# Performance work log

Measured on AMD Instinct MI355X. Metric: run time of the kernel, lower is better.

## Reference

```python
import jax, jax.numpy as jnp
import numpy as np

B, D, C = 16384, 512, 1000  # batch, feature dim, number of class prototypes


def setup_inputs() -> dict:
    key = jax.random.key(0)
    kx, kp = jax.random.split(key)
    x = jax.random.normal(kx, (B, D), dtype=jnp.float32)
    protomat = jax.random.normal(kp, (C, D), dtype=jnp.float32)
    return {"x": x, "protomat": protomat}


def reference(x, protomat):
    # Squared L2 distance from every sample to every prototype:
    # dist[b, c] = sum_d (x[b,d] - protomat[c,d])^2
    # materializing the [B, C, D] broadcast the original loop implies.
    x_sq = jnp.sum(x * x, axis=1, keepdims=True)            # [B, 1]
    p_sq = jnp.sum(protomat * protomat, axis=1)             # [C]
    cross = jnp.einsum('bd,cd->bc', x, protomat)            # [B, C]
    return x_sq + p_sq[None, :] - 2.0 * cross               # [B, C]
```

## Files before the change

### kernel.cpp

```cpp
#include <hip/hip_runtime.h>
#include <hip/hip_bf16.h>


#define B_ROWS 16384
#define D_K    512
#define C_COLS 1000
#define C_PAD  1024

#define BM 256
#define BN 256
#define BK 32
#define NK (D_K / BK)
#define NBUF 4
#define TILE_SH 16384

typedef __attribute__((ext_vector_type(8))) short short8;
typedef __attribute__((ext_vector_type(4))) float f32x4;

__device__ __forceinline__ unsigned short f2bf(float f) {
  unsigned u = __float_as_uint(f);
  u += 0x7fffu + ((u >> 16) & 1u);
  return (unsigned short)(u >> 16);
}

__device__ __forceinline__ void gload16(const void* g, void* l) {
  __builtin_amdgcn_global_load_lds(
      (const __attribute__((address_space(1))) unsigned int*)g,
      (__attribute__((address_space(3))) unsigned int*)l, 16, 0, 0);
}

__global__ __launch_bounds__(256) void prep_kernel(
    const float* __restrict__ x, const float* __restrict__ p,
    unsigned short* __restrict__ xb, unsigned short* __restrict__ pb,
    float* __restrict__ xsq, float* __restrict__ psq) {
  const int wave = threadIdx.x >> 6;
  const int lane = threadIdx.x & 63;
  const int row  = blockIdx.x * 4 + wave;
  const bool isx = row < B_ROWS;
  const int r2   = isx ? row : row - B_ROWS;

  float v[8];
  if (isx) {
    const float4* s = reinterpret_cast<const float4*>(x + (size_t)r2 * D_K + lane * 8);
    float4 a = s[0], b = s[1];
    v[0] = a.x; v[1] = a.y; v[2] = a.z; v[3] = a.w;
    v[4] = b.x; v[5] = b.y; v[6] = b.z; v[7] = b.w;
  } else if (r2 < C_COLS) {
    const float4* s = reinterpret_cast<const float4*>(p + (size_t)r2 * D_K + lane * 8);
    float4 a = s[0], b = s[1];
    v[0] = a.x; v[1] = a.y; v[2] = a.z; v[3] = a.w;
    v[4] = b.x; v[5] = b.y; v[6] = b.z; v[7] = b.w;
  } else {
#pragma unroll
    for (int j = 0; j < 8; ++j) v[j] = 0.0f;
  }

  float ss = 0.0f;
  unsigned short u[8];
#pragma unroll
  for (int j = 0; j < 8; ++j) { ss += v[j] * v[j]; u[j] = f2bf(v[j]); }

  uint4 pk;
  pk.x = (unsigned)u[0] | ((unsigned)u[1] << 16);
  pk.y = (unsigned)u[2] | ((unsigned)u[3] << 16);
  pk.z = (unsigned)u[4] | ((unsigned)u[5] << 16);
  pk.w = (unsigned)u[6] | ((unsigned)u[7] << 16);
  unsigned short* dst = (isx ? xb : pb) + (size_t)r2 * D_K + lane * 8;
  *reinterpret_cast<uint4*>(dst) = pk;

#pragma unroll
  for (int off = 32; off > 0; off >>= 1) ss += __shfl_down(ss, off);
  if (lane == 0) (isx ? xsq : psq)[r2] = ss;
}

__global__ __launch_bounds__(512, 2) void gemm_kernel(
    const unsigned short* __restrict__ xb, const unsigned short* __restrict__ pb,
    const float* __restrict__ xsq, const float* __restrict__ psq,
    float* __restrict__ out) {
  __shared__ __align__(16) unsigned short L[NBUF * TILE_SH];

  const int tid  = threadIdx.x;
  const int lane = tid & 63;
  const int wave = tid >> 6;
  const int wm   = wave >> 2;
  const int wn   = wave & 3;

  const int bid = blockIdx.x;
  const int tt  = (bid & 7) * 32 + (bid >> 3);
  const int bm  = tt >> 2;
  const int bn  = tt & 3;

  const int chA0 = tid, chA1 = tid + 512;
  const int rA0 = chA0 >> 2, rA1 = chA1 >> 2;
  const int ksA0 = ((chA0 & 3) - (rA0 >> 1)) & 3;
  const int ksA1 = ((chA1 & 3) - (rA1 >> 1)) & 3;
  const unsigned short* gA0 = xb + ((size_t)bm * BM + rA0) * D_K + ksA0 * 8;
  const unsigned short* gA1 = xb + ((size_t)bm * BM + rA1) * D_K + ksA1 * 8;
  const unsigned short* gB0 = pb + ((size_t)bn * BN + rA0) * D_K + ksA0 * 8;
  const unsigned short* gB1 = pb + ((size_t)bn * BN + rA1) * D_K + ksA1 * 8;
  unsigned short* lA0 = &L[chA0 * 8];
  unsigned short* lA1 = &L[chA1 * 8];
  unsigned short* lB0 = &L[8192 + chA0 * 8];
  unsigned short* lB1 = &L[8192 + chA1 * 8];

  f32x4 acc[8][4];
#pragma unroll
  for (int m = 0; m < 8; ++m)
#pragma unroll
    for (int n = 0; n < 4; ++n) acc[m][n] = (f32x4){0.f, 0.f, 0.f, 0.f};

  const int l15 = lane & 15;
  const int pos = (((lane >> 4) + (l15 >> 1)) & 3);
  const int rdA = (wm * 128 + l15) * 32 + pos * 8;
  const int rdB = 8192 + (wn * 64 + l15) * 32 + pos * 8;

#define STAGE(T, BUF)                                     \
  do {                                                    \
    const int ko = (T)*BK;                                \
    const int bo = (BUF)*TILE_SH;                         \
    gload16(gA0 + ko, lA0 + bo);                          \
    gload16(gA1 + ko, lA1 + bo);                          \
    gload16(gB0 + ko, lB0 + bo);                          \
    gload16(gB1 + ko, lB1 + bo);                          \
  } while (0)

#define COMPUTE(BUF)                                                          \
  do {                                                                        \
    const unsigned short* Ab = &L[(BUF)*TILE_SH] + rdA;                       \
    const unsigned short* Bb = &L[(BUF)*TILE_SH] + rdB;                       \
    short8 bfr[4];                                                            \
    _Pragma("unroll") for (int n = 0; n < 4; ++n)                             \
        bfr[n] = *reinterpret_cast<const short8*>(Bb + n * 512);              \
    __builtin_amdgcn_s_setprio(1);                                            \
    _Pragma("unroll") for (int m = 0; m < 8; ++m) {                           \
      short8 af = *reinterpret_cast<const short8*>(Ab + m * 512);             \
      _Pragma("unroll") for (int n = 0; n < 4; ++n)                           \
          acc[m][n] = __builtin_amdgcn_mfma_f32_16x16x32_bf16(                \
              af, bfr[n], acc[m][n], 0, 0, 0);                                \
    }                                                                         \
    __builtin_amdgcn_s_setprio(0);                                            \
  } while (0)

  STAGE(0, 0);
  STAGE(1, 1);
  STAGE(2, 2);

#pragma unroll 1
  for (int t = 0; t < NK - 3; ++t) {
    asm volatile("s_waitcnt vmcnt(8)" ::: "memory");
    __builtin_amdgcn_s_barrier();
    STAGE(t + 3, (t + 3) & 3);
    COMPUTE(t & 3);
  }
  asm volatile("s_waitcnt vmcnt(8)" ::: "memory");
  __builtin_amdgcn_s_barrier();
  COMPUTE(13 & 3);
  asm volatile("s_waitcnt vmcnt(4)" ::: "memory");
  __builtin_amdgcn_s_barrier();
  COMPUTE(14 & 3);
  asm volatile("s_waitcnt vmcnt(0)" ::: "memory");
  __builtin_amdgcn_s_barrier();
  COMPUTE(15 & 3);

#undef STAGE
#undef COMPUTE

  const int colb = bn * BN + wn * 64 + l15;
  float pc[4];
#pragma unroll
  for (int n = 0; n < 4; ++n) pc[n] = psq[colb + n * 16];

  const int rowb = bm * BM + wm * 128 + ((lane >> 4) << 2);
#pragma unroll
  for (int m = 0; m < 8; ++m) {
#pragma unroll
    for (int r = 0; r < 4; ++r) {
      const int row = rowb + m * 16 + r;
      const float xs = xsq[row];
#pragma unroll
      for (int n = 0; n < 4; ++n) {
        const int c = colb + n * 16;
        if (c < C_COLS)
          out[(size_t)row * C_COLS + c] = xs + pc[n] - 2.0f * acc[m][n][r];
      }
    }
  }
}

extern "C" void kernel_launch(void* const* d_in, const int* in_sizes, int n_in,
                              void* d_out, int out_size, void* d_ws, size_t ws_size,
                              hipStream_t stream) {
  const float* x = (const float*)d_in[0];
  const float* p = (const float*)d_in[1];
  float* out = (float*)d_out;

  char* ws = (char*)d_ws;
  unsigned short* xb  = (unsigned short*)ws;
  unsigned short* pb  = (unsigned short*)(ws + 16777216);
  float* xsq          = (float*)(ws + 16777216 + 1048576);
  float* psq          = (float*)(ws + 16777216 + 1048576 + 65536);

  prep_kernel<<<(B_ROWS + C_PAD) / 4, 256, 0, stream>>>(x, p, xb, pb, xsq, psq);

  gemm_kernel<<<256, 512, 0, stream>>>(xb, pb, xsq, psq, out);
}
```

Measured before the change: 111.1 us.

## Switch GEMM to 32x32x16 MFMA with two-pass 128-wide N tiles

Replaces the 16x16x32 bf16 MFMA tiling with 32x32x16 MFMAs, cutting per-wave accumulator state to four 16-float vectors. Each block now covers its 256-wide column range in two sequential 128-column passes, each with its own 4-stage LDS pipeline and epilogue. LDS per stage drops because the B tile is halved. The aim is fewer LDS fragment reads per flop and lower register pressure, at the cost of reloading the A tile from global memory in both passes and draining the pipeline twice per block.

New measurement: 119.8 us. 7.9% more time.

```diff
diff --git a/kernel.cpp b/kernel.cpp
--- a/kernel.cpp
+++ b/kernel.cpp
@@ -8,14 +8,16 @@
 #define C_PAD  1024
 
 #define BM 256
-#define BN 256
+#define BN 128
 #define BK 32
 #define NK (D_K / BK)
 #define NBUF 4
-#define TILE_SH 16384
+#define ABUF_SH 8192
+#define BBUF_SH 4096
+#define TILE_SH 12288
 
 typedef __attribute__((ext_vector_type(8))) short short8;
-typedef __attribute__((ext_vector_type(4))) float f32x4;
+typedef __attribute__((ext_vector_type(16))) float f32x16;
 
 __device__ __forceinline__ unsigned short f2bf(float f) {
   unsigned u = __float_as_uint(f);
@@ -82,8 +84,8 @@
   const int tid  = threadIdx.x;
   const int lane = tid & 63;
   const int wave = tid >> 6;
-  const int wm   = wave >> 2;
-  const int wn   = wave & 3;
+  const int wm   = wave >> 1;
+  const int wn   = wave & 1;
 
   const int bid = blockIdx.x;
   const int tt  = (bid & 7) * 32 + (bid >> 3);
@@ -91,99 +93,106 @@
   const int bn  = tt & 3;
 
   const int chA0 = tid, chA1 = tid + 512;
-  const int rA0 = chA0 >> 2, rA1 = chA1 >> 2;
+  const int rA0 = chA0 >> 2, rA1 = chA1 >> 2, rB = tid >> 2;
   const int ksA0 = ((chA0 & 3) - (rA0 >> 1)) & 3;
   const int ksA1 = ((chA1 & 3) - (rA1 >> 1)) & 3;
+  const int ksB  = ((tid & 3) - (rB >> 1)) & 3;
   const unsigned short* gA0 = xb + ((size_t)bm * BM + rA0) * D_K + ksA0 * 8;
   const unsigned short* gA1 = xb + ((size_t)bm * BM + rA1) * D_K + ksA1 * 8;
-  const unsigned short* gB0 = pb + ((size_t)bn * BN + rA0) * D_K + ksA0 * 8;
-  const unsigned short* gB1 = pb + ((size_t)bn * BN + rA1) * D_K + ksA1 * 8;
   unsigned short* lA0 = &L[chA0 * 8];
   unsigned short* lA1 = &L[chA1 * 8];
-  unsigned short* lB0 = &L[8192 + chA0 * 8];
-  unsigned short* lB1 = &L[8192 + chA1 * 8];
-
-  f32x4 acc[8][4];
-#pragma unroll
-  for (int m = 0; m < 8; ++m)
-#pragma unroll
-    for (int n = 0; n < 4; ++n) acc[m][n] = (f32x4){0.f, 0.f, 0.f, 0.f};
-
-  const int l15 = lane & 15;
-  const int pos = (((lane >> 4) + (l15 >> 1)) & 3);
-  const int rdA = (wm * 128 + l15) * 32 + pos * 8;
-  const int rdB = 8192 + (wn * 64 + l15) * 32 + pos * 8;
-
-#define STAGE(T, BUF)                                     \
-  do {                                                    \
-    const int ko = (T)*BK;                                \
-    const int bo = (BUF)*TILE_SH;                         \
-    gload16(gA0 + ko, lA0 + bo);                          \
-    gload16(gA1 + ko, lA1 + bo);                          \
-    gload16(gB0 + ko, lB0 + bo);                          \
-    gload16(gB1 + ko, lB1 + bo);                          \
-  } while (0)
-
-#define COMPUTE(BUF)                                                          \
-  do {                                                                        \
-    const unsigned short* Ab = &L[(BUF)*TILE_SH] + rdA;                       \
-    const unsigned short* Bb = &L[(BUF)*TILE_SH] + rdB;                       \
-    short8 bfr[4];                                                            \
-    _Pragma("unroll") for (int n = 0; n < 4; ++n)                             \
-        bfr[n] = *reinterpret_cast<const short8*>(Bb + n * 512);              \
-    __builtin_amdgcn_s_setprio(1);                                            \
-    _Pragma("unroll") for (int m = 0; m < 8; ++m) {                           \
-      short8 af = *reinterpret_cast<const short8*>(Ab + m * 512);             \
-      _Pragma("unroll") for (int n = 0; n < 4; ++n)                           \
-          acc[m][n] = __builtin_amdgcn_mfma_f32_16x16x32_bf16(                \
-              af, bfr[n], acc[m][n], 0, 0, 0);                                \
-    }                                                                         \
-    __builtin_amdgcn_s_setprio(0);                                            \
-  } while (0)
-
-  STAGE(0, 0);
-  STAGE(1, 1);
-  STAGE(2, 2);
+  unsigned short* lB0 = &L[ABUF_SH + tid * 8];
+
+  const int row_l = lane & 31;
+  const int pos   = (((lane >> 5) + (row_l >> 1)) & 3);
+  const int rdA0  = (wm * 64 + row_l) * 32 + pos * 8;
+  const int rdA1  = rdA0 ^ 16;
+  const int rdB0  = (wn * 64 + row_l) * 32 + pos * 8;
+  const int rdB1  = rdB0 ^ 16;
+
+  f32x16 acc0, acc1, acc2, acc3;
+  const unsigned short* gBp = nullptr;
+
+  auto STAGE = [&](int T, int BUF) {
+    const int ko = T * BK;
+    const int bo = BUF * TILE_SH;
+    gload16(gA0 + ko, lA0 + bo);
+    gload16(gA1 + ko, lA1 + bo);
+    gload16(gBp + ko, lB0 + bo);
+  };
+
+  auto COMPUTE = [&](int BUF) {
+    const unsigned short* Ab = &L[BUF * TILE_SH];
+    const unsigned short* Bb = Ab + ABUF_SH;
+    short8 a00 = *reinterpret_cast<const short8*>(Ab + rdA0);
+    short8 a01 = *reinterpret_cast<const short8*>(Ab + rdA1);
+    short8 a10 = *reinterpret_cast<const short8*>(Ab + rdA0 + 1024);
+    short8 a11 = *reinterpret_cast<const short8*>(Ab + rdA1 + 1024);
+    short8 b00 = *reinterpret_cast<const short8*>(Bb + rdB0);
+    short8 b01 = *reinterpret_cast<const short8*>(Bb + rdB1);
+    short8 b10 = *reinterpret_cast<const short8*>(Bb + rdB0 + 1024);
+    short8 b11 = *reinterpret_cast<const short8*>(Bb + rdB1 + 1024);
+    __builtin_amdgcn_s_setprio(1);
+    acc0 = __builtin_amdgcn_mfma_f32_32x32x16_bf16(a00, b00, acc0, 0, 0, 0);
+    acc0 = __builtin_amdgcn_mfma_f32_32x32x16_bf16(a01, b01, acc0, 0, 0, 0);
+    acc1 = __builtin_amdgcn_mfma_f32_32x32x16_bf16(a00, b10, acc1, 0, 0, 0);
+    acc1 = __builtin_amdgcn_mfma_f32_32x32x16_bf16(a01, b11, acc1, 0, 0, 0);
+    acc2 = __builtin_amdgcn_mfma_f32_32x32x16_bf16(a10, b00, acc2, 0, 0, 0);
+    acc2 = __builtin_amdgcn_mfma_f32_32x32x16_bf16(a11, b01, acc2, 0, 0, 0);
+    acc3 = __builtin_amdgcn_mfma_f32_32x32x16_bf16(a10, b10, acc3, 0, 0, 0);
+    acc3 = __builtin_amdgcn_mfma_f32_32x32x16_bf16(a11, b11, acc3, 0, 0, 0);
+    __builtin_amdgcn_s_setprio(0);
+  };
 
 #pragma unroll 1
-  for (int t = 0; t < NK - 3; ++t) {
-    asm volatile("s_waitcnt vmcnt(8)" ::: "memory");
+  for (int pass = 0; pass < 2; ++pass) {
+    const int bn2 = bn + 4 * pass;
+    gBp = pb + ((size_t)bn2 * BN + rB) * D_K + ksB * 8;
+
+    const f32x16 z = {0.f};
+    acc0 = z; acc1 = z; acc2 = z; acc3 = z;
+
+    STAGE(0, 0);
+    STAGE(1, 1);
+    STAGE(2, 2);
+
+#pragma unroll 1
+    for (int t = 0; t < NK - 3; ++t) {
+      asm volatile("s_waitcnt vmcnt(6)" ::: "memory");
+      __builtin_amdgcn_s_barrier();
+      STAGE(t + 3, (t + 3) & 3);
+      COMPUTE(t & 3);
+    }
+    asm volatile("s_waitcnt vmcnt(6)" ::: "memory");
     __builtin_amdgcn_s_barrier();
-    STAGE(t + 3, (t + 3) & 3);
-    COMPUTE(t & 3);
-  }
-  asm volatile("s_waitcnt vmcnt(8)" ::: "memory");
-  __builtin_amdgcn_s_barrier();
-  COMPUTE(13 & 3);
-  asm volatile("s_waitcnt vmcnt(4)" ::: "memory");
-  __builtin_amdgcn_s_barrier();
-  COMPUTE(14 & 3);
-  asm volatile("s_waitcnt vmcnt(0)" ::: "memory");
-  __builtin_amdgcn_s_barrier();
-  COMPUTE(15 & 3);
-
-#undef STAGE
-#undef COMPUTE
-
-  const int colb = bn * BN + wn * 64 + l15;
-  float pc[4];
-#pragma unroll
-  for (int n = 0; n < 4; ++n) pc[n] = psq[colb + n * 16];
-
-  const int rowb = bm * BM + wm * 128 + ((lane >> 4) << 2);
-#pragma unroll
-  for (int m = 0; m < 8; ++m) {
-#pragma unroll
-    for (int r = 0; r < 4; ++r) {
-      const int row = rowb + m * 16 + r;
-      const float xs = xsq[row];
-#pragma unroll
-      for (int n = 0; n < 4; ++n) {
-        const int c = colb + n * 16;
-        if (c < C_COLS)
-          out[(size_t)row * C_COLS + c] = xs + pc[n] - 2.0f * acc[m][n][r];
-      }
+    COMPUTE(1);
+    asm volatile("s_waitcnt vmcnt(3)" ::: "memory");
+    __builtin_amdgcn_s_barrier();
+    COMPUTE(2);
+    asm volatile("s_waitcnt vmcnt(0)" ::: "memory");
+    __builtin_amdgcn_s_barrier();
+    COMPUTE(3);
+
+    const int colb = bn2 * BN + wn * 64 + row_l;
+    const float pc0 = psq[colb];
+    const float pc1 = psq[colb + 32];
+    const int rowb = bm * BM + wm * 64 + ((lane >> 5) << 2);
+
+#define EPI(ACCL, ACCR, MM)                                                  \
+    _Pragma("unroll") for (int g = 0; g < 4; ++g) {                          \
+      _Pragma("unroll") for (int r = 0; r < 4; ++r) {                        \
+        const int reg = g * 4 + r;                                           \
+        const int row = rowb + (MM)*32 + g * 8 + r;                          \
+        const float xs = xsq[row];                                           \
+        if (colb < C_COLS)                                                   \
+          out[(size_t)row * C_COLS + colb] = xs + pc0 - 2.0f * ACCL[reg];    \
+        if (colb + 32 < C_COLS)                                              \
+          out[(size_t)row * C_COLS + colb + 32] = xs + pc1 - 2.0f * ACCR[reg];\
+      }                                                                      \
     }
+    EPI(acc0, acc1, 0)
+    EPI(acc2, acc3, 1)
+#undef EPI
   }
 }
 
```

## Restructure GEMM main loop into finer-grained phased pipeline with BK=64 double buffering

Applied to the files above, without the earlier changes.

Replaces the 4-deep BK=32 ring buffer with two BK=64 buffers, each split into two K-halves. Each K-half is processed in two M-half phases, and a quarter of the next tile's global-to-LDS loads is issued in every phase. The goal is finer interleaving of loads with MFMA work, in the style of ping-pong scheduling. The cost is two barriers per phase plus an lgkmcnt(0) wait, which could add synchronisation overhead.

After: 114.8 us. +3.4%, slower.

```diff
diff --git a/kernel.cpp b/kernel.cpp
--- a/kernel.cpp
+++ b/kernel.cpp
@@ -9,10 +9,8 @@
 
 #define BM 256
 #define BN 256
-#define BK 32
-#define NK (D_K / BK)
-#define NBUF 4
-#define TILE_SH 16384
+#define BK 64
+#define NT (D_K / BK)
 
 typedef __attribute__((ext_vector_type(8))) short short8;
 typedef __attribute__((ext_vector_type(4))) float f32x4;
@@ -27,6 +25,10 @@
   __builtin_amdgcn_global_load_lds(
       (const __attribute__((address_space(1))) unsigned int*)g,
       (__attribute__((address_space(3))) unsigned int*)l, 16, 0, 0);
+}
+
+__device__ __forceinline__ f32x4 MFMA(short8 a, short8 b, f32x4 c) {
+  return __builtin_amdgcn_mfma_f32_16x16x32_bf16(a, b, c, 0, 0, 0);
 }
 
 __global__ __launch_bounds__(256) void prep_kernel(
@@ -77,7 +79,8 @@
     const unsigned short* __restrict__ xb, const unsigned short* __restrict__ pb,
     const float* __restrict__ xsq, const float* __restrict__ psq,
     float* __restrict__ out) {
-  __shared__ __align__(16) unsigned short L[NBUF * TILE_SH];
+  __shared__ __align__(16) unsigned short L[65536];
+  unsigned short* Lp = L;
 
   const int tid  = threadIdx.x;
   const int lane = tid & 63;
@@ -90,18 +93,27 @@
   const int bm  = tt >> 2;
   const int bn  = tt & 3;
 
-  const int chA0 = tid, chA1 = tid + 512;
-  const int rA0 = chA0 >> 2, rA1 = chA1 >> 2;
-  const int ksA0 = ((chA0 & 3) - (rA0 >> 1)) & 3;
-  const int ksA1 = ((chA1 & 3) - (rA1 >> 1)) & 3;
-  const unsigned short* gA0 = xb + ((size_t)bm * BM + rA0) * D_K + ksA0 * 8;
-  const unsigned short* gA1 = xb + ((size_t)bm * BM + rA1) * D_K + ksA1 * 8;
-  const unsigned short* gB0 = pb + ((size_t)bn * BN + rA0) * D_K + ksA0 * 8;
-  const unsigned short* gB1 = pb + ((size_t)bn * BN + rA1) * D_K + ksA1 * 8;
-  unsigned short* lA0 = &L[chA0 * 8];
-  unsigned short* lA1 = &L[chA1 * 8];
-  unsigned short* lB0 = &L[8192 + chA0 * 8];
-  unsigned short* lB1 = &L[8192 + chA1 * 8];
+  const int r_s  = tid >> 2;
+  const int ks_s = ((tid & 3) - (r_s >> 1)) & 3;
+  const unsigned short* gA = xb + ((size_t)bm * BM + r_s) * D_K + ks_s * 8;
+  const unsigned short* gB = pb + ((size_t)bn * BN + r_s) * D_K + ks_s * 8;
+
+#define STAGE_A(T, H)                                                        \
+  do {                                                                       \
+    const int off_ = (T) * 64 + (H) * 32;                                    \
+    unsigned short* d_ = Lp + (((T) & 1) * 32768 + (H) * 8192 + tid * 8);    \
+    gload16(gA + off_, d_);                                                  \
+    gload16(gA + off_ + 65536, d_ + 4096);                                   \
+  } while (0)
+
+#define STAGE_B(T, H)                                                        \
+  do {                                                                       \
+    const int off_ = (T) * 64 + (H) * 32;                                    \
+    unsigned short* d_ =                                                     \
+        Lp + (((T) & 1) * 32768 + 16384 + (H) * 8192 + tid * 8);             \
+    gload16(gB + off_, d_);                                                  \
+    gload16(gB + off_ + 65536, d_ + 4096);                                   \
+  } while (0)
 
   f32x4 acc[8][4];
 #pragma unroll
@@ -109,61 +121,83 @@
 #pragma unroll
     for (int n = 0; n < 4; ++n) acc[m][n] = (f32x4){0.f, 0.f, 0.f, 0.f};
 
-  const int l15 = lane & 15;
-  const int pos = (((lane >> 4) + (l15 >> 1)) & 3);
-  const int rdA = (wm * 128 + l15) * 32 + pos * 8;
-  const int rdB = 8192 + (wn * 64 + l15) * 32 + pos * 8;
-
-#define STAGE(T, BUF)                                     \
-  do {                                                    \
-    const int ko = (T)*BK;                                \
-    const int bo = (BUF)*TILE_SH;                         \
-    gload16(gA0 + ko, lA0 + bo);                          \
-    gload16(gA1 + ko, lA1 + bo);                          \
-    gload16(gB0 + ko, lB0 + bo);                          \
-    gload16(gB1 + ko, lB1 + bo);                          \
+  const int l15  = lane & 15;
+  const int posL = (((lane >> 4) + (l15 >> 1)) & 3);
+  const int rdA  = (wm * 128 + l15) * 32 + posL * 8;
+  const int rdB  = 16384 + (wn * 64 + l15) * 32 + posL * 8;
+
+  short8 bF0, bF1, bF2, bF3;
+
+#define VM8  asm volatile("s_waitcnt vmcnt(8)" ::: "memory")
+#define VM4  asm volatile("s_waitcnt vmcnt(4)" ::: "memory")
+#define VM0  asm volatile("s_waitcnt vmcnt(0)" ::: "memory")
+#define NOVM (void)0
+
+#define PH(BUF, H, MH, STAGE_STMT, VM_STMT)                                   \
+  do {                                                                        \
+    STAGE_STMT;                                                               \
+    VM_STMT;                                                                  \
+    asm volatile("" ::: "memory");                                            \
+    __builtin_amdgcn_s_barrier();                                             \
+    const unsigned short* Ap_ =                                               \
+        Lp + (BUF) * 32768 + (H) * 8192 + rdA + (MH) * 2048;                  \
+    short8 aF0 = *reinterpret_cast<const short8*>(Ap_ + 0);                   \
+    short8 aF1 = *reinterpret_cast<const short8*>(Ap_ + 512);                 \
+    short8 aF2 = *reinterpret_cast<const short8*>(Ap_ + 1024);                \
+    short8 aF3 = *reinterpret_cast<const short8*>(Ap_ + 1536);                \
+    if ((MH) == 0) {                                                          \
+      const unsigned short* Bp_ = Lp + (BUF) * 32768 + (H) * 8192 + rdB;      \
+      bF0 = *reinterpret_cast<const short8*>(Bp_ + 0);                        \
+      bF1 = *reinterpret_cast<const short8*>(Bp_ + 512);                      \
+      bF2 = *reinterpret_cast<const short8*>(Bp_ + 1024);                     \
+      bF3 = *reinterpret_cast<const short8*>(Bp_ + 1536);                     \
+    }                                                                         \
+    __builtin_amdgcn_s_setprio(1);                                            \
+    acc[(MH)*4+0][0] = MFMA(aF0, bF0, acc[(MH)*4+0][0]);                      \
+    acc[(MH)*4+0][1] = MFMA(aF0, bF1, acc[(MH)*4+0][1]);                      \
+    acc[(MH)*4+0][2] = MFMA(aF0, bF2, acc[(MH)*4+0][2]);                      \
+    acc[(MH)*4+0][3] = MFMA(aF0, bF3, acc[(MH)*4+0][3]);                      \
+    acc[(MH)*4+1][0] = MFMA(aF1, bF0, acc[(MH)*4+1][0]);                      \
+    acc[(MH)*4+1][1] = MFMA(aF1, bF1, acc[(MH)*4+1][1]);                      \
+    acc[(MH)*4+1][2] = MFMA(aF1, bF2, acc[(MH)*4+1][2]);                      \
+    acc[(MH)*4+1][3] = MFMA(aF1, bF3, acc[(MH)*4+1][3]);                      \
+    acc[(MH)*4+2][0] = MFMA(aF2, bF0, acc[(MH)*4+2][0]);                      \
+    acc[(MH)*4+2][1] = MFMA(aF2, bF1, acc[(MH)*4+2][1]);                      \
+    acc[(MH)*4+2][2] = MFMA(aF2, bF2, acc[(MH)*4+2][2]);                      \
+    acc[(MH)*4+2][3] = MFMA(aF2, bF3, acc[(MH)*4+2][3]);                      \
+    acc[(MH)*4+3][0] = MFMA(aF3, bF0, acc[(MH)*4+3][0]);                      \
+    acc[(MH)*4+3][1] = MFMA(aF3, bF1, acc[(MH)*4+3][1]);                      \
+    acc[(MH)*4+3][2] = MFMA(aF3, bF2, acc[(MH)*4+3][2]);                      \
+    acc[(MH)*4+3][3] = MFMA(aF3, bF3, acc[(MH)*4+3][3]);                      \
+    __builtin_amdgcn_s_setprio(0);                                            \
+    asm volatile("s_waitcnt lgkmcnt(0)" ::: "memory");                        \
+    __builtin_amdgcn_s_barrier();                                             \
   } while (0)
 
-#define COMPUTE(BUF)                                                          \
-  do {                                                                        \
-    const unsigned short* Ab = &L[(BUF)*TILE_SH] + rdA;                       \
-    const unsigned short* Bb = &L[(BUF)*TILE_SH] + rdB;                       \
-    short8 bfr[4];                                                            \
-    _Pragma("unroll") for (int n = 0; n < 4; ++n)                             \
-        bfr[n] = *reinterpret_cast<const short8*>(Bb + n * 512);              \
-    __builtin_amdgcn_s_setprio(1);                                            \
-    _Pragma("unroll") for (int m = 0; m < 8; ++m) {                           \
-      short8 af = *reinterpret_cast<const short8*>(Ab + m * 512);             \
-      _Pragma("unroll") for (int n = 0; n < 4; ++n)                           \
-          acc[m][n] = __builtin_amdgcn_mfma_f32_16x16x32_bf16(                \
-              af, bfr[n], acc[m][n], 0, 0, 0);                                \
-    }                                                                         \
-    __builtin_amdgcn_s_setprio(0);                                            \
-  } while (0)
-
-  STAGE(0, 0);
-  STAGE(1, 1);
-  STAGE(2, 2);
+  STAGE_A(0, 0); STAGE_B(0, 0);
+  STAGE_A(0, 1); STAGE_B(0, 1);
+  STAGE_A(1, 0); STAGE_B(1, 0);
 
 #pragma unroll 1
-  for (int t = 0; t < NK - 3; ++t) {
-    asm volatile("s_waitcnt vmcnt(8)" ::: "memory");
-    __builtin_amdgcn_s_barrier();
-    STAGE(t + 3, (t + 3) & 3);
-    COMPUTE(t & 3);
+  for (int T = 0; T < 6; ++T) {
+    const int c = T & 1;
+    PH(c, 0, 0, STAGE_A(T + 1, 1), VM8);
+    PH(c, 0, 1, STAGE_B(T + 1, 1), NOVM);
+    PH(c, 1, 0, STAGE_A(T + 2, 0), VM8);
+    PH(c, 1, 1, STAGE_B(T + 2, 0), NOVM);
   }
-  asm volatile("s_waitcnt vmcnt(8)" ::: "memory");
-  __builtin_amdgcn_s_barrier();
-  COMPUTE(13 & 3);
-  asm volatile("s_waitcnt vmcnt(4)" ::: "memory");
-  __builtin_amdgcn_s_barrier();
-  COMPUTE(14 & 3);
-  asm volatile("s_waitcnt vmcnt(0)" ::: "memory");
-  __builtin_amdgcn_s_barrier();
-  COMPUTE(15 & 3);
-
-#undef STAGE
-#undef COMPUTE
+  PH(0, 0, 0, STAGE_A(7, 1), VM8);
+  PH(0, 0, 1, STAGE_B(7, 1), NOVM);
+  PH(0, 1, 0, NOVM, VM8);
+  PH(0, 1, 1, NOVM, NOVM);
+  PH(1, 0, 0, NOVM, VM4);
+  PH(1, 0, 1, NOVM, NOVM);
+  PH(1, 1, 0, NOVM, VM0);
+  PH(1, 1, 1, NOVM, NOVM);
+
+#undef PH
+#undef STAGE_A
+#undef STAGE_B
 
   const int colb = bn * BN + wn * 64 + l15;
   float pc[4];
```

## Shrink GEMM tile to 256x128 with triple buffering and more blocks

Applied to the files above, without the earlier changes.

Halves the N tile to 128 and regroups 8 waves as a 4x2 grid, each holding 4x4 accumulators. Buffering drops from four stages to three and launch bounds target four blocks per CU, with 512 blocks launched instead of 256, so more waves stay resident on the 256-CU part. The aim is better occupancy and latency hiding, paid for with lower operand reuse per block and more A-tile traffic.

Measured after the change: 111.1 us. No clear change (+0.1%).

```diff
diff --git a/kernel.cpp b/kernel.cpp
--- a/kernel.cpp
+++ b/kernel.cpp
@@ -8,11 +8,12 @@
 #define C_PAD  1024
 
 #define BM 256
-#define BN 256
+#define BN 128
 #define BK 32
 #define NK (D_K / BK)
-#define NBUF 4
-#define TILE_SH 16384
+#define NBUF 3
+#define ABUF_SH 8192
+#define TILE_SH 12288
 
 typedef __attribute__((ext_vector_type(8))) short short8;
 typedef __attribute__((ext_vector_type(4))) float f32x4;
@@ -27,6 +28,10 @@
   __builtin_amdgcn_global_load_lds(
       (const __attribute__((address_space(1))) unsigned int*)g,
       (__attribute__((address_space(3))) unsigned int*)l, 16, 0, 0);
+}
+
+__device__ __forceinline__ f32x4 MFMA(short8 a, short8 b, f32x4 c) {
+  return __builtin_amdgcn_mfma_f32_16x16x32_bf16(a, b, c, 0, 0, 0);
 }
 
 __global__ __launch_bounds__(256) void prep_kernel(
@@ -73,7 +78,7 @@
   if (lane == 0) (isx ? xsq : psq)[r2] = ss;
 }
 
-__global__ __launch_bounds__(512, 2) void gemm_kernel(
+__global__ __launch_bounds__(512, 4) void gemm_kernel(
     const unsigned short* __restrict__ xb, const unsigned short* __restrict__ pb,
     const float* __restrict__ xsq, const float* __restrict__ psq,
     float* __restrict__ out) {
@@ -82,37 +87,35 @@
   const int tid  = threadIdx.x;
   const int lane = tid & 63;
   const int wave = tid >> 6;
-  const int wm   = wave >> 2;
-  const int wn   = wave & 3;
+  const int wm   = wave >> 1;
+  const int wn   = wave & 1;
 
   const int bid = blockIdx.x;
-  const int tt  = (bid & 7) * 32 + (bid >> 3);
-  const int bm  = tt >> 2;
-  const int bn  = tt & 3;
-
-  const int chA0 = tid, chA1 = tid + 512;
-  const int rA0 = chA0 >> 2, rA1 = chA1 >> 2;
-  const int ksA0 = ((chA0 & 3) - (rA0 >> 1)) & 3;
-  const int ksA1 = ((chA1 & 3) - (rA1 >> 1)) & 3;
+  const int tt  = (bid & 7) * 64 + (bid >> 3);
+  const int bm  = tt >> 3;
+  const int bn  = tt & 7;
+
+  const int rA0 = tid >> 2, rA1 = rA0 + 128, rB = tid >> 2;
+  const int ksA0 = ((tid & 3) - (rA0 >> 1)) & 3;
+  const int ksA1 = (((tid + 512) & 3) - (rA1 >> 1)) & 3;
+  const int ksB  = ((tid & 3) - (rB >> 1)) & 3;
   const unsigned short* gA0 = xb + ((size_t)bm * BM + rA0) * D_K + ksA0 * 8;
   const unsigned short* gA1 = xb + ((size_t)bm * BM + rA1) * D_K + ksA1 * 8;
-  const unsigned short* gB0 = pb + ((size_t)bn * BN + rA0) * D_K + ksA0 * 8;
-  const unsigned short* gB1 = pb + ((size_t)bn * BN + rA1) * D_K + ksA1 * 8;
-  unsigned short* lA0 = &L[chA0 * 8];
-  unsigned short* lA1 = &L[chA1 * 8];
-  unsigned short* lB0 = &L[8192 + chA0 * 8];
-  unsigned short* lB1 = &L[8192 + chA1 * 8];
-
-  f32x4 acc[8][4];
-#pragma unroll
-  for (int m = 0; m < 8; ++m)
+  const unsigned short* gB  = pb + ((size_t)bn * BN + rB) * D_K + ksB * 8;
+  unsigned short* lA0 = &L[tid * 8];
+  unsigned short* lA1 = &L[(tid + 512) * 8];
+  unsigned short* lB  = &L[ABUF_SH + tid * 8];
+
+  f32x4 acc[4][4];
+#pragma unroll
+  for (int m = 0; m < 4; ++m)
 #pragma unroll
     for (int n = 0; n < 4; ++n) acc[m][n] = (f32x4){0.f, 0.f, 0.f, 0.f};
 
-  const int l15 = lane & 15;
-  const int pos = (((lane >> 4) + (l15 >> 1)) & 3);
-  const int rdA = (wm * 128 + l15) * 32 + pos * 8;
-  const int rdB = 8192 + (wn * 64 + l15) * 32 + pos * 8;
+  const int l15  = lane & 15;
+  const int posL = (((lane >> 4) + (l15 >> 1)) & 3);
+  const int rdA  = (wm * 64 + l15) * 32 + posL * 8;
+  const int rdB  = ABUF_SH + (wn * 64 + l15) * 32 + posL * 8;
 
 #define STAGE(T, BUF)                                     \
   do {                                                    \
@@ -120,8 +123,7 @@
     const int bo = (BUF)*TILE_SH;                         \
     gload16(gA0 + ko, lA0 + bo);                          \
     gload16(gA1 + ko, lA1 + bo);                          \
-    gload16(gB0 + ko, lB0 + bo);                          \
-    gload16(gB1 + ko, lB1 + bo);                          \
+    gload16(gB + ko, lB + bo);                            \
   } while (0)
 
 #define COMPUTE(BUF)                                                          \
@@ -132,35 +134,30 @@
     _Pragma("unroll") for (int n = 0; n < 4; ++n)                             \
         bfr[n] = *reinterpret_cast<const short8*>(Bb + n * 512);              \
     __builtin_amdgcn_s_setprio(1);                                            \
-    _Pragma("unroll") for (int m = 0; m < 8; ++m) {                           \
+    _Pragma("unroll") for (int m = 0; m < 4; ++m) {                           \
       short8 af = *reinterpret_cast<const short8*>(Ab + m * 512);             \
       _Pragma("unroll") for (int n = 0; n < 4; ++n)                           \
-          acc[m][n] = __builtin_amdgcn_mfma_f32_16x16x32_bf16(                \
-              af, bfr[n], acc[m][n], 0, 0, 0);                                \
+          acc[m][n] = MFMA(af, bfr[n], acc[m][n]);                            \
     }                                                                         \
     __builtin_amdgcn_s_setprio(0);                                            \
   } while (0)
 
   STAGE(0, 0);
   STAGE(1, 1);
-  STAGE(2, 2);
-
-#pragma unroll 1
-  for (int t = 0; t < NK - 3; ++t) {
-    asm volatile("s_waitcnt vmcnt(8)" ::: "memory");
+
+#pragma unroll
+  for (int t = 0; t < NK - 2; ++t) {
+    asm volatile("s_waitcnt vmcnt(3)" ::: "memory");
     __builtin_amdgcn_s_barrier();
-    STAGE(t + 3, (t + 3) & 3);
-    COMPUTE(t & 3);
+    STAGE(t + 2, (t + 2) % 3);
+    COMPUTE(t % 3);
   }
-  asm volatile("s_waitcnt vmcnt(8)" ::: "memory");
+  asm volatile("s_waitcnt vmcnt(3)" ::: "memory");
   __builtin_amdgcn_s_barrier();
-  COMPUTE(13 & 3);
-  asm volatile("s_waitcnt vmcnt(4)" ::: "memory");
-  __builtin_amdgcn_s_barrier();
-  COMPUTE(14 & 3);
+  COMPUTE(14 % 3);
   asm volatile("s_waitcnt vmcnt(0)" ::: "memory");
   __builtin_amdgcn_s_barrier();
-  COMPUTE(15 & 3);
+  COMPUTE(15 % 3);
 
 #undef STAGE
 #undef COMPUTE
@@ -170,9 +167,9 @@
 #pragma unroll
   for (int n = 0; n < 4; ++n) pc[n] = psq[colb + n * 16];
 
-  const int rowb = bm * BM + wm * 128 + ((lane >> 4) << 2);
-#pragma unroll
-  for (int m = 0; m < 8; ++m) {
+  const int rowb = bm * BM + wm * 64 + ((lane >> 4) << 2);
+#pragma unroll
+  for (int m = 0; m < 4; ++m) {
 #pragma unroll
     for (int r = 0; r < 4; ++r) {
       const int row = rowb + m * 16 + r;
@@ -202,5 +199,5 @@
 
   prep_kernel<<<(B_ROWS + C_PAD) / 4, 256, 0, stream>>>(x, p, xb, pb, xsq, psq);
 
-  gemm_kernel<<<256, 512, 0, stream>>>(xb, pb, xsq, psq, out);
-}
+  gemm_kernel<<<512, 512, 0, stream>>>(xb, pb, xsq, psq, out);
+}
```
